# Kernel tuning notes

Measured on AMD Instinct MI355X. Metric: run time of the kernel, lower is better.

Reference implementation:

```python
import jax, jax.numpy as jnp
import numpy as np
from math import sqrt

HEADS = 16
DIM_HEAD = 64
BETA = 1.0 / sqrt(DIM_HEAD)


def setup_inputs() -> dict:
    key = jax.random.key(0)
    k1, k2, k3 = jax.random.split(key, 3)
    b, n, dim = 2, 2048, 1024
    inner = HEADS * DIM_HEAD  # 1024
    x = jax.random.normal(k1, (b, n, dim), dtype=jnp.float32)
    W_qk = jax.random.normal(k2, (dim, 2 * inner), dtype=jnp.float32) * 0.02
    W_out = jax.random.normal(k3, (inner, dim), dtype=jnp.float32) * 0.02
    return {"x": x, "W_qk": W_qk, "W_out": W_out}


def reference(x, W_qk, W_out):
    # x: [b, n, dim]; to_qk: Linear(dim, 2*inner, bias=False)
    b, n, _ = x.shape
    qk = x @ W_qk                                   # [b, n, 2*inner]
    q, k = jnp.split(qk, 2, axis=-1)                # each [b, n, inner]
    # b n (h d) -> b h n d
    q = q.reshape(b, n, HEADS, DIM_HEAD).transpose(0, 2, 1, 3)
    k = k.reshape(b, n, HEADS, DIM_HEAD).transpose(0, 2, 1, 3)
    # beta-scaled scores
    scores = jnp.einsum('bhid,bhjd->bhij', q * BETA, k)  # [b, h, n, n]
    mask_value = -jnp.finfo(scores.dtype).max
    causal_mask = jnp.triu(jnp.ones((n, n), dtype=bool), k=1)
    scores = jnp.where(causal_mask, mask_value, scores)
    attn = jax.nn.softmax(scores, axis=-1)
    # K is reused as V
    out = jnp.einsum('bhij,bhjd->bhid', attn, k)    # [b, h, n, d]
    out = out.transpose(0, 2, 1, 3).reshape(b, n, HEADS * DIM_HEAD)
    # to_out Linear (dropout is identity in eval)
    return out @ W_out
```

## Files before the change

kernel.cpp:

```cpp
#include <hip/hip_runtime.h>
#include <hip/hip_bf16.h>
#include <math.h>

typedef short bf16x8 __attribute__((ext_vector_type(8)));
typedef float f32x4 __attribute__((ext_vector_type(4)));

__device__ __forceinline__ float bf2f(unsigned short u) {
    return __uint_as_float(((unsigned int)u) << 16);
}
__device__ __forceinline__ unsigned short f2bf(float f) {
    unsigned int u = __float_as_uint(f);
    u = (u + 0x7FFFu + ((u >> 16) & 1u)) >> 16;
    return (unsigned short)u;
}
__device__ __forceinline__ unsigned int pk2bf(float a, float b) {
    __hip_bfloat162 u = __float22bfloat162_rn(make_float2(a, b));
    return *(unsigned int*)&u;
}

#define ASYNC16(gp, lp)                                                        \
    __builtin_amdgcn_global_load_lds(                                          \
        (const __attribute__((address_space(1))) unsigned int*)(gp),           \
        (__attribute__((address_space(3))) unsigned int*)(lp), 16, 0, 0)

__global__ __launch_bounds__(256) void prep_kernel(const float* __restrict__ x,
                                                   const float* __restrict__ Wqk,
                                                   const float* __restrict__ Wout,
                                                   unsigned short* __restrict__ xb,
                                                   unsigned short* __restrict__ Wqk_t,
                                                   unsigned short* __restrict__ Wout_t) {
    __shared__ float tile[32][33];
    const int bid = blockIdx.x;
    const int tid = threadIdx.x;

    if (bid < 2048) {
        const int i = (bid * 256 + tid) * 8;
        float4 a = *(const float4*)(x + i);
        float4 b = *(const float4*)(x + i + 4);
        bf16x8 v;
        v[0] = (short)f2bf(a.x); v[1] = (short)f2bf(a.y); v[2] = (short)f2bf(a.z); v[3] = (short)f2bf(a.w);
        v[4] = (short)f2bf(b.x); v[5] = (short)f2bf(b.y); v[6] = (short)f2bf(b.z); v[7] = (short)f2bf(b.w);
        *(bf16x8*)(xb + i) = v;
        return;
    }

    const float* in;
    unsigned short* out;
    int K, N, t;
    if (bid < 4096) { t = bid - 2048; in = Wqk;  out = Wqk_t;  K = 1024; N = 2048; }
    else            { t = bid - 4096; in = Wout; out = Wout_t; K = 1024; N = 1024; }
    const int k0 = (t & 31) * 32, n0 = (t >> 5) * 32;
    const int tx = tid & 31, ty = tid >> 5;
    #pragma unroll
    for (int i = ty; i < 32; i += 8)
        tile[i][tx] = in[(size_t)(k0 + i) * N + (n0 + tx)];
    __syncthreads();
    #pragma unroll
    for (int i = ty; i < 32; i += 8)
        out[(size_t)(n0 + i) * K + (k0 + tx)] = f2bf(tile[tx][i]);
}

__global__ __launch_bounds__(256) void ktrans_kernel(const unsigned short* __restrict__ qkb,
                                                     unsigned short* __restrict__ kT) {
    __shared__ unsigned short tl[64][68];
    const int b = blockIdx.z;
    const int tok0 = blockIdx.x * 64;
    const int f0 = blockIdx.y * 64;
    const int r = threadIdx.x >> 4;
    const int c = (threadIdx.x & 15) * 4;
    #pragma unroll
    for (int i = 0; i < 4; ++i) {
        const int rr = r + 16 * i;
        ushort4 v = *(const ushort4*)(qkb + ((size_t)(b * 2048 + tok0 + rr)) * 2048 + 1024 + f0 + c);
        *(ushort4*)&tl[rr][c] = v;
    }
    __syncthreads();
    #pragma unroll
    for (int i = 0; i < 4; ++i) {
        const int fr = r + 16 * i;
        ushort4 v;
        v.x = tl[c + 0][fr]; v.y = tl[c + 1][fr]; v.z = tl[c + 2][fr]; v.w = tl[c + 3][fr];
        *(ushort4*)(kT + ((size_t)(b * 1024 + f0 + fr)) * 2048 + tok0 + c) = v;
    }
}

template <bool STORE_BF16, bool WRITE_KT>
__global__ __launch_bounds__(256) void gemm64k_kernel(const unsigned short* __restrict__ A,
                                                      const unsigned short* __restrict__ Bt,
                                                      void* __restrict__ C,
                                                      unsigned short* __restrict__ kTout,
                                                      int K, int lda, int ldb, int ldc) {
    __shared__ unsigned short smem[64 * 64 + 128 * 64];
    unsigned short* As = smem;
    unsigned short* Bs = smem + 64 * 64;
    const int tid = threadIdx.x;
    const int wave = tid >> 6;
    const int lane = tid & 63;
    const int quad = lane >> 4;
    const int col  = lane & 15;
    const int sw   = col & 7;
    const int wm = (wave >> 1) * 32;
    const int wn = (wave & 1) * 64;
    const int m0 = blockIdx.x * 64, n0 = blockIdx.y * 128;

    f32x4 acc[2][4];
    #pragma unroll
    for (int i = 0; i < 2; ++i)
        #pragma unroll
        for (int j = 0; j < 4; ++j) { acc[i][j][0] = 0.f; acc[i][j][1] = 0.f; acc[i][j][2] = 0.f; acc[i][j][3] = 0.f; }

    const int r8 = lane >> 3;
    const int c8 = (lane & 7) ^ r8;

    for (int k0 = 0; k0 < K; k0 += 64) {
        __syncthreads();
        const unsigned short* ga = A  + (size_t)(m0 + wave * 8 + r8) * lda + k0 + c8 * 8;
        const unsigned short* gb = Bt + (size_t)(n0 + wave * 8 + r8) * ldb + k0 + c8 * 8;
        ASYNC16(ga,            &As[(wave * 8) * 64]);
        ASYNC16(ga + 32 * lda, &As[(32 + wave * 8) * 64]);
        ASYNC16(gb,            &Bs[(wave * 8) * 64]);
        ASYNC16(gb + 32 * ldb, &Bs[(32 + wave * 8) * 64]);
        ASYNC16(gb + 64 * ldb, &Bs[(64 + wave * 8) * 64]);
        ASYNC16(gb + 96 * ldb, &Bs[(96 + wave * 8) * 64]);
        __syncthreads();

        bf16x8 af[2][2], bf[4][2];
        #pragma unroll
        for (int mf = 0; mf < 2; ++mf) {
            const int base = (wm + mf * 16 + col) * 64;
            af[mf][0] = *(const bf16x8*)&As[base + ((quad    ) ^ sw) * 8];
            af[mf][1] = *(const bf16x8*)&As[base + ((quad + 4) ^ sw) * 8];
        }
        #pragma unroll
        for (int nf = 0; nf < 4; ++nf) {
            const int base = (wn + nf * 16 + col) * 64;
            bf[nf][0] = *(const bf16x8*)&Bs[base + ((quad    ) ^ sw) * 8];
            bf[nf][1] = *(const bf16x8*)&Bs[base + ((quad + 4) ^ sw) * 8];
        }
        #pragma unroll
        for (int mf = 0; mf < 2; ++mf)
            #pragma unroll
            for (int nf = 0; nf < 4; ++nf) {
                acc[mf][nf] = __builtin_amdgcn_mfma_f32_16x16x32_bf16(af[mf][0], bf[nf][0], acc[mf][nf], 0, 0, 0);
                acc[mf][nf] = __builtin_amdgcn_mfma_f32_16x16x32_bf16(af[mf][1], bf[nf][1], acc[mf][nf], 0, 0, 0);
            }
    }

    #pragma unroll
    for (int mf = 0; mf < 2; ++mf) {
        const int row0 = m0 + wm + mf * 16 + quad * 4;
        #pragma unroll
        for (int nf = 0; nf < 4; ++nf) {
            const int cc = n0 + wn + nf * 16 + col;
            #pragma unroll
            for (int r = 0; r < 4; ++r) {
                if (STORE_BF16)
                    ((unsigned short*)C)[(size_t)(row0 + r) * ldc + cc] = f2bf(acc[mf][nf][r]);
                else
                    ((float*)C)[(size_t)(row0 + r) * ldc + cc] = acc[mf][nf][r];
            }
        }
    }

    if (WRITE_KT && n0 >= 1024) {
        __syncthreads();
        unsigned short* tt = smem;
        #pragma unroll
        for (int mf = 0; mf < 2; ++mf)
            #pragma unroll
            for (int nf = 0; nf < 4; ++nf)
                #pragma unroll
                for (int r = 0; r < 4; ++r)
                    tt[(wn + nf * 16 + col) * 68 + (wm + mf * 16 + quad * 4 + r)] =
                        f2bf(acc[mf][nf][r]);
        __syncthreads();
        const int b = m0 >> 11, token0 = m0 & 2047, f0 = n0 - 1024;
        const int f = tid >> 1, half = tid & 1;
        unsigned short* kout =
            kTout + ((size_t)(b * 1024 + f0 + f)) * 2048 + token0 + half * 32;
        #pragma unroll
        for (int j = 0; j < 8; ++j)
            *(ushort4*)(kout + j * 4) = *(const ushort4*)&tt[f * 68 + half * 32 + j * 4];
    }
}

__global__ __launch_bounds__(256, 4) void attn_v16_kernel(const unsigned short* __restrict__ qkb,
                                                          const unsigned short* __restrict__ kT,
                                                          unsigned short* __restrict__ aout) {
    __shared__ unsigned short Kbuf[2][2][64 * 64];
    __shared__ unsigned short Ps[4][16 * 64];

    const int bh = blockIdx.x;
    const int b = bh >> 4, h = bh & 15;
    const int qtile = 31 - (int)blockIdx.y;
    const int tid = threadIdx.x;
    const int wave = tid >> 6, lane = tid & 63, quad = lane >> 4, col = lane & 15;
    const int sw = col & 7;

    bf16x8 qa0, qa1;
    {
        const unsigned short* qp =
            qkb + ((size_t)(b * 2048 + qtile * 64 + wave * 16 + col)) * 2048 + h * 64;
        bf16x8 r0 = *(const bf16x8*)(qp + quad * 8);
        bf16x8 r1 = *(const bf16x8*)(qp + 32 + quad * 8);
        const float sc = 0.125f * 1.44269504088896f;
        #pragma unroll
        for (int i = 0; i < 8; ++i) {
            qa0[i] = (short)f2bf(bf2f((unsigned short)r0[i]) * sc);
            qa1[i] = (short)f2bf(bf2f((unsigned short)r1[i]) * sc);
        }
    }

    bf16x8 ones;
    #pragma unroll
    for (int i = 0; i < 8; ++i) ones[i] = (short)0x3F80;

    f32x4 accO[4];
    #pragma unroll
    for (int t = 0; t < 4; ++t) { accO[t][0] = 0.f; accO[t][1] = 0.f; accO[t][2] = 0.f; accO[t][3] = 0.f; }
    f32x4 accL = {0.f, 0.f, 0.f, 0.f};

    bf16x8 pa0p = {}, pa1p = {};
    bf16x8 vlo[4] = {}, vhi[4] = {};

    const int r8 = lane >> 3;
    const int c8 = (lane & 7) ^ r8;
    const unsigned short* knp =
        qkb + ((size_t)(b * 2048 + wave * 16 + r8)) * 2048 + 1024 + h * 64 + c8 * 8;
    const unsigned short* ktp = kT + ((size_t)(bh * 64 + wave * 16 + r8)) * 2048 + c8 * 8;

    auto issue = [&](int jt, int p) {
        const unsigned short* kn = knp + (size_t)jt * 64 * 2048;
        const unsigned short* kt = ktp + jt * 64;
        unsigned short* knl = &Kbuf[p][0][(wave * 16) * 64];
        unsigned short* ktl = &Kbuf[p][1][(wave * 16) * 64];
        ASYNC16(kn,            knl);
        ASYNC16(kn + 8 * 2048, knl + 8 * 64);
        ASYNC16(kt,            ktl);
        ASYNC16(kt + 8 * 2048, ktl + 8 * 64);
    };

    issue(0, 0);

    for (int jt = 0; jt <= qtile; ++jt) {
        const int cur = jt & 1;
        __builtin_amdgcn_s_barrier();
        if (jt < qtile) issue(jt + 1, cur ^ 1);
        if (jt < qtile) __builtin_amdgcn_s_waitcnt(0xF74);
        else            __builtin_amdgcn_s_waitcnt(0xF70);
        __builtin_amdgcn_s_barrier();
        __asm__ volatile("" ::: "memory");

        const unsigned short* Knc = &Kbuf[cur][0][0];
        const unsigned short* Ktc = &Kbuf[cur][1][0];

        const bool diag = (jt == qtile);
        const int tmax = diag ? wave : 3;

        f32x4 c[4];
        __builtin_amdgcn_s_setprio(1);
        #pragma unroll
        for (int t = 0; t < 4; ++t) {
            if (t <= tmax) {
                const int row = (t * 16 + col) * 64;
                bf16x8 ka0 = *(const bf16x8*)&Knc[row + (quad ^ sw) * 8];
                bf16x8 ka1 = *(const bf16x8*)&Knc[row + ((4 + quad) ^ sw) * 8];
                f32x4 ci = {-16.f, -16.f, -16.f, -16.f};
                ci = __builtin_amdgcn_mfma_f32_16x16x32_bf16(ka0, qa0, ci, 0, 0, 0);
                ci = __builtin_amdgcn_mfma_f32_16x16x32_bf16(ka1, qa1, ci, 0, 0, 0);
                c[t] = ci;
            }
        }
        if (jt) {
            #pragma unroll
            for (int t = 0; t < 4; ++t) {
                accO[t] = __builtin_amdgcn_mfma_f32_16x16x32_bf16(pa0p, vlo[t], accO[t], 0, 0, 0);
                accO[t] = __builtin_amdgcn_mfma_f32_16x16x32_bf16(pa1p, vhi[t], accO[t], 0, 0, 0);
            }
            accL = __builtin_amdgcn_mfma_f32_16x16x32_bf16(pa0p, ones, accL, 0, 0, 0);
            accL = __builtin_amdgcn_mfma_f32_16x16x32_bf16(pa1p, ones, accL, 0, 0, 0);
        }
        __builtin_amdgcn_s_setprio(0);

        unsigned int pw[4][2];
        #pragma unroll
        for (int t = 0; t < 4; ++t) {
            if (t <= tmax) {
                f32x4 ci = c[t];
                if (diag && t == wave) {
                    #pragma unroll
                    for (int r = 0; r < 4; ++r)
                        if (quad * 4 + r > col) ci[r] = -1e30f;
                }
                const float p0 = exp2f(ci[0]);
                const float p1 = exp2f(ci[1]);
                const float p2 = exp2f(ci[2]);
                const float p3 = exp2f(ci[3]);
                pw[t][0] = pk2bf(p0, p1);
                pw[t][1] = pk2bf(p2, p3);
            } else {
                pw[t][0] = 0u; pw[t][1] = 0u;
            }
        }

        unsigned short* psb = &Ps[wave][col * 64];
        #pragma unroll
        for (int t = 0; t < 4; ++t)
            *(uint2*)(psb + ((2 * t + (quad >> 1)) ^ sw) * 8 + (quad & 1) * 4) =
                make_uint2(pw[t][0], pw[t][1]);

        pa0p = *(const bf16x8*)(psb + (quad ^ sw) * 8);
        pa1p = *(const bf16x8*)(psb + ((4 + quad) ^ sw) * 8);

        #pragma unroll
        for (int t = 0; t < 4; ++t) {
            const int row = (t * 16 + col) * 64;
            vlo[t] = *(const bf16x8*)&Ktc[row + (quad ^ sw) * 8];
            vhi[t] = *(const bf16x8*)&Ktc[row + ((4 + quad) ^ sw) * 8];
        }
        __asm__ volatile("s_waitcnt lgkmcnt(0)" ::: "memory");
        __builtin_amdgcn_sched_barrier(0);
    }

    #pragma unroll
    for (int t = 0; t < 4; ++t) {
        accO[t] = __builtin_amdgcn_mfma_f32_16x16x32_bf16(pa0p, vlo[t], accO[t], 0, 0, 0);
        accO[t] = __builtin_amdgcn_mfma_f32_16x16x32_bf16(pa1p, vhi[t], accO[t], 0, 0, 0);
    }
    accL = __builtin_amdgcn_mfma_f32_16x16x32_bf16(pa0p, ones, accL, 0, 0, 0);
    accL = __builtin_amdgcn_mfma_f32_16x16x32_bf16(pa1p, ones, accL, 0, 0, 0);

    #pragma unroll
    for (int r = 0; r < 4; ++r) {
        const float inv = 1.f / accL[r];
        const size_t row = (size_t)b * 2048 + qtile * 64 + wave * 16 + quad * 4 + r;
        unsigned short* op = aout + row * 1024 + h * 64;
        op[col]      = f2bf(accO[0][r] * inv);
        op[16 + col] = f2bf(accO[1][r] * inv);
        op[32 + col] = f2bf(accO[2][r] * inv);
        op[48 + col] = f2bf(accO[3][r] * inv);
    }
}

extern "C" void kernel_launch(void* const* d_in, const int* in_sizes, int n_in,
                              void* d_out, int out_size, void* d_ws, size_t ws_size,
                              hipStream_t stream) {
    (void)in_sizes; (void)n_in; (void)out_size;
    const float* x    = (const float*)d_in[0];
    const float* Wqk  = (const float*)d_in[1];
    const float* Wout = (const float*)d_in[2];
    float* out = (float*)d_out;

    unsigned short* xb     = (unsigned short*)d_ws;
    unsigned short* Wqk_t  = xb     + (size_t)4096 * 1024;
    unsigned short* Wout_t = Wqk_t  + (size_t)2048 * 1024;
    unsigned short* qkb    = Wout_t + (size_t)1024 * 1024;
    unsigned short* aoutb  = qkb    + (size_t)4096 * 2048;
    unsigned short* kT_new = aoutb  + (size_t)4096 * 1024;

    const bool fused_kt = ws_size >= (size_t)46 * 1024 * 1024;
    unsigned short* kT = fused_kt ? kT_new : xb;

    prep_kernel<<<dim3(5120), dim3(256), 0, stream>>>(x, Wqk, Wout, xb, Wqk_t, Wout_t);

    if (fused_kt) {
        gemm64k_kernel<true, true><<<dim3(64, 16), dim3(256), 0, stream>>>(
            xb, Wqk_t, (void*)qkb, kT, 1024, 1024, 1024, 2048);
    } else {
        gemm64k_kernel<true, false><<<dim3(64, 16), dim3(256), 0, stream>>>(
            xb, Wqk_t, (void*)qkb, nullptr, 1024, 1024, 1024, 2048);
        ktrans_kernel<<<dim3(32, 16, 2), dim3(256), 0, stream>>>(qkb, kT);
    }

    attn_v16_kernel<<<dim3(32, 32), dim3(256), 0, stream>>>(qkb, kT, aoutb);

    gemm64k_kernel<false, false><<<dim3(64, 8), dim3(256), 0, stream>>>(
        aoutb, Wout_t, (void*)out, nullptr, 1024, 1024, 1024, 1024);
}
```

Measured before the change: 161.5 us.

## Reorder attention PV MMAs before QK and add smaller-tile output GEMM

Inside the attention loop, the deferred P·V MFMAs now issue before the QK score MFMAs. The V fragment LDS reads are issued right after them, so they overlap the softmax exp work, and the final wait is relaxed to lgkmcnt(2). The output projection switches from the 64-wide-K gemm kernel to a new 64x64-tile GEMM launched on a 64x16 grid, doubling the block count to improve CU occupancy. The relaxed waitcnt depends on exact LDS op ordering and could risk correctness, and the smaller tiles reduce data reuse.

```diff
diff --git a/kernel.cpp b/kernel.cpp
--- a/kernel.cpp
+++ b/kernel.cpp
@@ -184,7 +184,82 @@
     }
 }
 
-__global__ __launch_bounds__(256, 4) void attn_v16_kernel(const unsigned short* __restrict__ qkb,
+template <bool STORE_BF16>
+__global__ __launch_bounds__(256) void gemm64x64_kernel(const unsigned short* __restrict__ A,
+                                                        const unsigned short* __restrict__ Bt,
+                                                        void* __restrict__ C,
+                                                        int K, int lda, int ldb, int ldc) {
+    __shared__ unsigned short As[64 * 64];
+    __shared__ unsigned short Bs[64 * 64];
+    const int tid = threadIdx.x;
+    const int wave = tid >> 6;
+    const int lane = tid & 63;
+    const int quad = lane >> 4;
+    const int col  = lane & 15;
+    const int sw   = col & 7;
+    const int wm = (wave >> 1) * 32;
+    const int wn = (wave & 1) * 32;
+    const int m0 = blockIdx.x * 64, n0 = blockIdx.y * 64;
+
+    f32x4 acc[2][2];
+    #pragma unroll
+    for (int i = 0; i < 2; ++i)
+        #pragma unroll
+        for (int j = 0; j < 2; ++j) { acc[i][j][0] = 0.f; acc[i][j][1] = 0.f; acc[i][j][2] = 0.f; acc[i][j][3] = 0.f; }
+
+    const int r8 = lane >> 3;
+    const int c8 = (lane & 7) ^ r8;
+
+    for (int k0 = 0; k0 < K; k0 += 64) {
+        __syncthreads();
+        const unsigned short* ga = A  + (size_t)(m0 + wave * 8 + r8) * lda + k0 + c8 * 8;
+        const unsigned short* gb = Bt + (size_t)(n0 + wave * 8 + r8) * ldb + k0 + c8 * 8;
+        ASYNC16(ga,            &As[(wave * 8) * 64]);
+        ASYNC16(ga + 32 * lda, &As[(32 + wave * 8) * 64]);
+        ASYNC16(gb,            &Bs[(wave * 8) * 64]);
+        ASYNC16(gb + 32 * ldb, &Bs[(32 + wave * 8) * 64]);
+        __syncthreads();
+
+        bf16x8 af[2][2], bfr[2][2];
+        #pragma unroll
+        for (int mf = 0; mf < 2; ++mf) {
+            const int base = (wm + mf * 16 + col) * 64;
+            af[mf][0] = *(const bf16x8*)&As[base + ((quad    ) ^ sw) * 8];
+            af[mf][1] = *(const bf16x8*)&As[base + ((quad + 4) ^ sw) * 8];
+        }
+        #pragma unroll
+        for (int nf = 0; nf < 2; ++nf) {
+            const int base = (wn + nf * 16 + col) * 64;
+            bfr[nf][0] = *(const bf16x8*)&Bs[base + ((quad    ) ^ sw) * 8];
+            bfr[nf][1] = *(const bf16x8*)&Bs[base + ((quad + 4) ^ sw) * 8];
+        }
+        #pragma unroll
+        for (int mf = 0; mf < 2; ++mf)
+            #pragma unroll
+            for (int nf = 0; nf < 2; ++nf) {
+                acc[mf][nf] = __builtin_amdgcn_mfma_f32_16x16x32_bf16(af[mf][0], bfr[nf][0], acc[mf][nf], 0, 0, 0);
+                acc[mf][nf] = __builtin_amdgcn_mfma_f32_16x16x32_bf16(af[mf][1], bfr[nf][1], acc[mf][nf], 0, 0, 0);
+            }
+    }
+
+    #pragma unroll
+    for (int mf = 0; mf < 2; ++mf) {
+        const int row0 = m0 + wm + mf * 16 + quad * 4;
+        #pragma unroll
+        for (int nf = 0; nf < 2; ++nf) {
+            const int cc = n0 + wn + nf * 16 + col;
+            #pragma unroll
+            for (int r = 0; r < 4; ++r) {
+                if (STORE_BF16)
+                    ((unsigned short*)C)[(size_t)(row0 + r) * ldc + cc] = f2bf(acc[mf][nf][r]);
+                else
+                    ((float*)C)[(size_t)(row0 + r) * ldc + cc] = acc[mf][nf][r];
+            }
+        }
+    }
+}
+
+__global__ __launch_bounds__(256, 4) void attn_v18_kernel(const unsigned short* __restrict__ qkb,
                                                           const unsigned short* __restrict__ kT,
                                                           unsigned short* __restrict__ aout) {
     __shared__ unsigned short Kbuf[2][2][64 * 64];
@@ -257,8 +332,18 @@
         const bool diag = (jt == qtile);
         const int tmax = diag ? wave : 3;
 
+        __builtin_amdgcn_s_setprio(1);
+        if (jt) {
+            #pragma unroll
+            for (int t = 0; t < 4; ++t) {
+                accO[t] = __builtin_amdgcn_mfma_f32_16x16x32_bf16(pa0p, vlo[t], accO[t], 0, 0, 0);
+                accO[t] = __builtin_amdgcn_mfma_f32_16x16x32_bf16(pa1p, vhi[t], accO[t], 0, 0, 0);
+            }
+            accL = __builtin_amdgcn_mfma_f32_16x16x32_bf16(pa0p, ones, accL, 0, 0, 0);
+            accL = __builtin_amdgcn_mfma_f32_16x16x32_bf16(pa1p, ones, accL, 0, 0, 0);
+        }
+
         f32x4 c[4];
-        __builtin_amdgcn_s_setprio(1);
         #pragma unroll
         for (int t = 0; t < 4; ++t) {
             if (t <= tmax) {
@@ -271,16 +356,15 @@
                 c[t] = ci;
             }
         }
-        if (jt) {
-            #pragma unroll
-            for (int t = 0; t < 4; ++t) {
-                accO[t] = __builtin_amdgcn_mfma_f32_16x16x32_bf16(pa0p, vlo[t], accO[t], 0, 0, 0);
-                accO[t] = __builtin_amdgcn_mfma_f32_16x16x32_bf16(pa1p, vhi[t], accO[t], 0, 0, 0);
-            }
-            accL = __builtin_amdgcn_mfma_f32_16x16x32_bf16(pa0p, ones, accL, 0, 0, 0);
-            accL = __builtin_amdgcn_mfma_f32_16x16x32_bf16(pa1p, ones, accL, 0, 0, 0);
-        }
         __builtin_amdgcn_s_setprio(0);
+
+        #pragma unroll
+        for (int t = 0; t < 4; ++t) {
+            const int row = (t * 16 + col) * 64;
+            vlo[t] = *(const bf16x8*)&Ktc[row + (quad ^ sw) * 8];
+            vhi[t] = *(const bf16x8*)&Ktc[row + ((4 + quad) ^ sw) * 8];
+        }
+        __builtin_amdgcn_sched_barrier(0);
 
         unsigned int pw[4][2];
         #pragma unroll
@@ -312,13 +396,7 @@
         pa0p = *(const bf16x8*)(psb + (quad ^ sw) * 8);
         pa1p = *(const bf16x8*)(psb + ((4 + quad) ^ sw) * 8);
 
-        #pragma unroll
-        for (int t = 0; t < 4; ++t) {
-            const int row = (t * 16 + col) * 64;
-            vlo[t] = *(const bf16x8*)&Ktc[row + (quad ^ sw) * 8];
-            vhi[t] = *(const bf16x8*)&Ktc[row + ((4 + quad) ^ sw) * 8];
-        }
-        __asm__ volatile("s_waitcnt lgkmcnt(0)" ::: "memory");
+        __asm__ volatile("s_waitcnt lgkmcnt(2)" ::: "memory");
         __builtin_amdgcn_sched_barrier(0);
     }
 
@@ -372,8 +450,8 @@
         ktrans_kernel<<<dim3(32, 16, 2), dim3(256), 0, stream>>>(qkb, kT);
     }
 
-    attn_v16_kernel<<<dim3(32, 32), dim3(256), 0, stream>>>(qkb, kT, aoutb);
-
-    gemm64k_kernel<false, false><<<dim3(64, 8), dim3(256), 0, stream>>>(
-        aoutb, Wout_t, (void*)out, nullptr, 1024, 1024, 1024, 1024);
-}
+    attn_v18_kernel<<<dim3(32, 32), dim3(256), 0, stream>>>(qkb, kT, aoutb);
+
+    gemm64x64_kernel<false><<<dim3(64, 16), dim3(256), 0, stream>>>(
+        aoutb, Wout_t, (void*)out, 1024, 1024, 1024, 1024);
+}
```

Result: no change. 162.0 us (+0.3%).
